# Kernel optimization log

Hardware: AMD Instinct MI355X
Metric: run time of the kernel (lower is better)

The kernel has to match this reference:

```python
import jax, jax.numpy as jnp
import numpy as np

SEQ = 2048
D_MODEL = 2048
N_HEADS = 16
D_HEAD = D_MODEL // N_HEADS
GN_EPS = 1e-5


def apply_xpos(x, inv=False, base=10000.0, scale_base=512.0):
    # x: (sqlen, d_head). Standard xPos: rotary embedding with exponential length scale.
    s, d = x.shape
    half = d // 2
    freqs = 1.0 / (base ** (jnp.arange(half, dtype=jnp.float32) / half))
    pos = jnp.arange(s, dtype=jnp.float32)
    ang = pos[:, None] * freqs[None, :]                       # (s, half)
    sin, cos = jnp.sin(ang), jnp.cos(ang)
    scale = ((jnp.arange(half, dtype=jnp.float32) + 0.4 * d) / (1.4 * d)) ** (pos[:, None] / scale_base)
    if inv:
        scale = 1.0 / scale
    x1, x2 = x[:, :half], x[:, half:]
    y1 = (x1 * cos - x2 * sin) * scale
    y2 = (x1 * sin + x2 * cos) * scale
    return jnp.concatenate([y1, y2], axis=-1)


def setup_inputs() -> dict:
    key = jax.random.key(0)
    ks = jax.random.split(key, 8)
    s = D_MODEL ** -0.5
    return {
        "x": jax.random.normal(ks[0], (SEQ, D_MODEL), jnp.float32),
        "state": jax.random.normal(ks[1], (N_HEADS, D_HEAD, D_HEAD), jnp.float32) * 0.1,
        "Wqkv": jax.random.normal(ks[2], (3 * D_MODEL, D_MODEL), jnp.float32) * s,
        "Walpha": jax.random.normal(ks[3], (1, D_MODEL), jnp.float32) * s,
        "gn_w": jnp.ones((D_MODEL,), jnp.float32),
        "gn_b": jnp.zeros((D_MODEL,), jnp.float32),
        "Wgate": jax.random.normal(ks[4], (D_MODEL, D_MODEL), jnp.float32) * s,
        "Wout": jax.random.normal(ks[5], (D_MODEL, D_MODEL), jnp.float32) * s,
    }


def reference(x, state, Wqkv, Walpha, gn_w, gn_b, Wgate, Wout):
    sqlen = x.shape[0]
    # qkv projection -> (3, H, s, Dh)
    qkv = (x @ Wqkv.T).reshape(sqlen, 3, N_HEADS, D_HEAD).transpose(1, 2, 0, 3)
    q, k, v = qkv[0], qkv[1], qkv[2]
    q = jax.vmap(apply_xpos)(q)
    k = jax.vmap(lambda t: apply_xpos(t, inv=True))(k)

    alphas = -jnp.log1p(jnp.exp(-(x @ Walpha.T)))             # log-sigmoid, (s, 1)
    k = (1.0 - jnp.exp(alphas)) * k                            # broadcast (s,1) over (H,s,Dh)
    a = jnp.cumsum(alphas, axis=0)                             # (s, 1)

    # Decay matrix; mask BEFORE exp (equivalent to tril-after since upper is zeroed,
    # but avoids overflow in exp for the upper triangle).
    tril = jnp.tril(jnp.ones((sqlen, sqlen), bool))
    Delta = jnp.exp(jnp.where(tril, a - a.T, -jnp.inf))        # (s, s)

    attn = jnp.tril(jnp.einsum('hid,hjd,ij->hij', q, k, Delta))  # (H, s, s)
    ret = jnp.einsum('hij,hjd->ihd', attn, v)                    # (s, H, Dh)

    new_state = jnp.exp(a[-1]) * state                           # (H, Dh, Dh)
    ret = ret + jnp.einsum('hid,hde->ihe', q, new_state)
    new_state = new_state + jnp.einsum('hid,hie,i->hde', k, v, jnp.exp(a[::-1, 0]))

    # GroupNorm(n_heads groups) over d_model, per token
    r = ret.reshape(sqlen, N_HEADS, D_HEAD)
    mu = r.mean(-1, keepdims=True)
    var = r.var(-1, keepdims=True)
    r = (r - mu) * jax.lax.rsqrt(var + GN_EPS)
    ret = r.reshape(sqlen, D_MODEL) * gn_w + gn_b

    gate = jax.nn.swish(ret @ Wgate.T)
    out = (gate * ret) @ Wout.T
    return out, new_state
```

## Files before the change

kernel.cpp:

```cpp
#include <hip/hip_runtime.h>

#define SEQ 2048
#define DM 2048
#define NH 16
#define DH 128

typedef float f32x4 __attribute__((ext_vector_type(4)));
typedef short s16x8 __attribute__((ext_vector_type(8)));

__device__ __forceinline__ ushort f2bf(float f) {
    unsigned u = __builtin_bit_cast(unsigned, f);
    return (ushort)((u + 0x7FFFu + ((u >> 16) & 1u)) >> 16);
}
__device__ __forceinline__ float bf2f(ushort u) {
    return __builtin_bit_cast(float, (unsigned)u << 16);
}
__device__ __forceinline__ void gload_lds16(const void* g, void* l) {
    __builtin_amdgcn_global_load_lds((const __attribute__((address_space(1))) void*)g,
                                     (__attribute__((address_space(3))) void*)l, 16, 0, 0);
}

__global__ __launch_bounds__(256) void k_cvt_bf16(const float* __restrict__ in,
                                                  ushort* __restrict__ out, int n4) {
    int i = blockIdx.x * 256 + threadIdx.x;
    if (i < n4) {
        float4 v = ((const float4*)in)[i];
        ushort4 o;
        o.x = f2bf(v.x); o.y = f2bf(v.y); o.z = f2bf(v.z); o.w = f2bf(v.w);
        ((ushort4*)out)[i] = o;
    }
}

__global__ __launch_bounds__(256) void k_cvt_dual(const float* __restrict__ in0,
                                                  ushort* __restrict__ out0,
                                                  const float* __restrict__ in1,
                                                  ushort* __restrict__ out1, int n4) {
    int i = blockIdx.x * 256 + threadIdx.x;
    if (i >= n4) return;
    const float* in = blockIdx.y ? in1 : in0;
    ushort* out = blockIdx.y ? out1 : out0;
    float4 v = ((const float4*)in)[i];
    ushort4 o;
    o.x = f2bf(v.x); o.y = f2bf(v.y); o.z = f2bf(v.z); o.w = f2bf(v.w);
    ((ushort4*)out)[i] = o;
}

__global__ __launch_bounds__(256) void k_xprep(const float* __restrict__ x,
                                               const float* __restrict__ wal,
                                               ushort* __restrict__ x_bf,
                                               float* __restrict__ z) {
    int row = blockIdx.x, t = threadIdx.x;
    const float4* xr = (const float4*)(x + (size_t)row * DM);
    const float4* wa = (const float4*)wal;
    float4 v0 = xr[t], v1 = xr[t + 256];
    float4 w0 = wa[t], w1 = wa[t + 256];
    float s = v0.x * w0.x + v0.y * w0.y + v0.z * w0.z + v0.w * w0.w
            + v1.x * w1.x + v1.y * w1.y + v1.z * w1.z + v1.w * w1.w;
    ushort4 o0, o1;
    o0.x = f2bf(v0.x); o0.y = f2bf(v0.y); o0.z = f2bf(v0.z); o0.w = f2bf(v0.w);
    o1.x = f2bf(v1.x); o1.y = f2bf(v1.y); o1.z = f2bf(v1.z); o1.w = f2bf(v1.w);
    ushort4* xb = (ushort4*)(x_bf + (size_t)row * DM);
    xb[t] = o0; xb[t + 256] = o1;
    __shared__ float red[4];
    int lane = t & 63, wv = t >> 6;
    #pragma unroll
    for (int off = 32; off; off >>= 1) s += __shfl_down(s, off);
    if (lane == 0) red[wv] = s;
    __syncthreads();
    if (t == 0) z[row] = red[0] + red[1] + red[2] + red[3];
}

__global__ __launch_bounds__(256) void k_scan(const float* __restrict__ z,
                                              float* __restrict__ a,
                                              float* __restrict__ wrev,
                                              float* __restrict__ kscale,
                                              float* __restrict__ exp_alast) {
    __shared__ float sh[SEQ];
    __shared__ float csum[256];
    int t = threadIdx.x;
    for (int i = t; i < SEQ; i += 256) {
        float al = -log1pf(expf(-z[i]));
        sh[i] = al;
        kscale[i] = 1.f - expf(al);
    }
    __syncthreads();
    int base = t * 8;
    float run = 0.f, loc[8];
    #pragma unroll
    for (int j = 0; j < 8; j++) { run += sh[base + j]; loc[j] = run; }
    csum[t] = run;
    __syncthreads();
    if (t == 0) {
        float r = 0.f;
        for (int i = 0; i < 256; i++) { float v = csum[i]; csum[i] = r; r += v; }
    }
    __syncthreads();
    float off = csum[t];
    #pragma unroll
    for (int j = 0; j < 8; j++) { float av = loc[j] + off; sh[base + j] = av; a[base + j] = av; }
    __syncthreads();
    for (int i = t; i < SEQ; i += 256) wrev[i] = expf(sh[SEQ - 1 - i]);
    if (t == 0) *exp_alast = expf(sh[SEQ - 1]);
}

__global__ __launch_bounds__(256) void k_trig(float* __restrict__ tsin,
                                              float* __restrict__ tcos,
                                              float* __restrict__ tsc) {
    int idx = blockIdx.x * 256 + threadIdx.x;
    int i = idx >> 6, j = idx & 63;
    float freq = powf(10000.f, -(float)j / 64.f);
    float ang = (float)i * freq;
    tsin[idx] = sinf(ang);
    tcos[idx] = cosf(ang);
    tsc[idx]  = powf(((float)j + 51.2f) / 179.2f, (float)i / 512.f);
}

template <int EPI, int STORE_BF16>
__global__ __launch_bounds__(256) void k_gemm_mfma(
    const ushort* __restrict__ A,
    const ushort* __restrict__ B,
    void* __restrict__ Cv, int ldc,
    const ushort* __restrict__ aux,
    int K)
{
    __shared__ __align__(16) ushort As[128 * 32];
    __shared__ __align__(16) ushort Bs[128 * 32];
    int bx = blockIdx.x, by = blockIdx.y;
    int nwg = gridDim.x * gridDim.y;
    if ((nwg & 7) == 0) {
        int id = by * gridDim.x + bx;
        int cpx = nwg >> 3;
        int swz = (id & 7) * cpx + (id >> 3);
        bx = swz % gridDim.x; by = swz / gridDim.x;
    }
    int bm = by * 128, bn = bx * 128;
    int tid = threadIdx.x;
    int w = tid >> 6, l = tid & 63;
    int wr = w >> 1, wc = w & 1;
    int lr = l & 15, kg = l >> 4;

    int srow = w * 16 + (l >> 2);
    int scol = (l & 3) * 8;
    const ushort* ga0 = A + (size_t)(bm + srow) * K + scol;
    const ushort* ga1 = A + (size_t)(bm + 64 + srow) * K + scol;
    const ushort* gb0 = B + (size_t)(bn + srow) * K + scol;
    const ushort* gb1 = B + (size_t)(bn + 64 + srow) * K + scol;
    ushort* la0 = As + w * 512;
    ushort* la1 = As + 2048 + w * 512;
    ushort* lb0 = Bs + w * 512;
    ushort* lb1 = Bs + 2048 + w * 512;

    f32x4 acc[4][4] = {};

    for (int k0 = 0; k0 < K; k0 += 32) {
        __syncthreads();
        gload_lds16(ga0 + k0, la0);
        gload_lds16(ga1 + k0, la1);
        gload_lds16(gb0 + k0, lb0);
        gload_lds16(gb1 + k0, lb1);
        __syncthreads();

        s16x8 af[4], bfr[4];
        #pragma unroll
        for (int m = 0; m < 4; m++)
            af[m] = *(const s16x8*)(As + (wr * 64 + m * 16 + lr) * 32 + kg * 8);
        #pragma unroll
        for (int n = 0; n < 4; n++)
            bfr[n] = *(const s16x8*)(Bs + (wc * 64 + n * 16 + lr) * 32 + kg * 8);
        #pragma unroll
        for (int m = 0; m < 4; m++)
            #pragma unroll
            for (int n = 0; n < 4; n++)
                asm volatile("v_mfma_f32_16x16x32_bf16 %0, %1, %2, %0"
                             : "+v"(acc[m][n]) : "v"(af[m]), "v"(bfr[n]));
    }
    asm volatile("s_nop 7\n\ts_nop 7\n\ts_nop 7" ::: );

    #pragma unroll
    for (int m = 0; m < 4; m++) {
        int grow = bm + wr * 64 + m * 16 + kg * 4;
        #pragma unroll
        for (int n = 0; n < 4; n++) {
            int gcol = bn + wc * 64 + n * 16 + lr;
            #pragma unroll
            for (int j = 0; j < 4; j++) {
                float c = acc[m][n][j];
                size_t off = (size_t)(grow + j) * ldc + gcol;
                if (EPI == 1) {
                    float sig = 1.f / (1.f + __expf(-c));
                    c = c * sig * bf2f(aux[off]);
                }
                if (STORE_BF16) ((ushort*)Cv)[off] = f2bf(c);
                else            ((float*)Cv)[off] = c;
            }
        }
    }
}

__global__ __launch_bounds__(256) void k_gemm_qkv(
    const ushort* __restrict__ A,
    const ushort* __restrict__ B,
    const float* __restrict__ tsin,
    const float* __restrict__ tcos,
    const float* __restrict__ tsc,
    const float* __restrict__ kscale,
    const float* __restrict__ wrev,
    ushort* __restrict__ qh,
    ushort* __restrict__ kh,
    ushort* __restrict__ vth,
    ushort* __restrict__ kwtr)
{
    __shared__ __align__(16) char smem[34816];
    ushort* As = (ushort*)smem;
    ushort* Bs = (ushort*)(smem + 8192);
    const int K = DM;
    int bx = blockIdx.x, by = blockIdx.y;
    {
        int id = by * gridDim.x + bx;
        int cpx = (gridDim.x * gridDim.y) >> 3;
        int swz = (id & 7) * cpx + (id >> 3);
        bx = swz % gridDim.x; by = swz / gridDim.x;
    }
    int bm = by * 128, bn = bx * 128;
    int tid = threadIdx.x;
    int w = tid >> 6, l = tid & 63;
    int wr = w >> 1, wc = w & 1;
    int lr = l & 15, kg = l >> 4;

    int srow = w * 16 + (l >> 2);
    int scol = (l & 3) * 8;
    const ushort* ga0 = A + (size_t)(bm + srow) * K + scol;
    const ushort* ga1 = A + (size_t)(bm + 64 + srow) * K + scol;
    const ushort* gb0 = B + (size_t)(bn + srow) * K + scol;
    const ushort* gb1 = B + (size_t)(bn + 64 + srow) * K + scol;
    ushort* la0 = As + w * 512;
    ushort* la1 = As + 2048 + w * 512;
    ushort* lb0 = Bs + w * 512;
    ushort* lb1 = Bs + 2048 + w * 512;

    f32x4 acc[4][4] = {};

    for (int k0 = 0; k0 < K; k0 += 32) {
        __syncthreads();
        gload_lds16(ga0 + k0, la0);
        gload_lds16(ga1 + k0, la1);
        gload_lds16(gb0 + k0, lb0);
        gload_lds16(gb1 + k0, lb1);
        __syncthreads();

        s16x8 af[4], bfr[4];
        #pragma unroll
        for (int m = 0; m < 4; m++)
            af[m] = *(const s16x8*)(As + (wr * 64 + m * 16 + lr) * 32 + kg * 8);
        #pragma unroll
        for (int n = 0; n < 4; n++)
            bfr[n] = *(const s16x8*)(Bs + (wc * 64 + n * 16 + lr) * 32 + kg * 8);
        #pragma unroll
        for (int m = 0; m < 4; m++)
            #pragma unroll
            for (int n = 0; n < 4; n++)
                asm volatile("v_mfma_f32_16x16x32_bf16 %0, %1, %2, %0"
                             : "+v"(acc[m][n]) : "v"(af[m]), "v"(bfr[n]));
    }
    asm volatile("s_nop 7\n\ts_nop 7\n\ts_nop 7" ::: );

    __syncthreads();
    ushort* S = (ushort*)smem;
    #pragma unroll
    for (int m = 0; m < 4; m++) {
        int row = wr * 64 + m * 16 + kg * 4;
        #pragma unroll
        for (int n = 0; n < 4; n++) {
            int col = wc * 64 + n * 16 + lr;
            #pragma unroll
            for (int j = 0; j < 4; j++)
                S[(row + j) * 129 + col] = f2bf(acc[m][n][j]);
        }
    }
    __syncthreads();

    int type = bn >> 11;
    int h = (bn & 2047) >> 7;

    if (type < 2) {
        #pragma unroll 4
        for (int rr = 0; rr < 32; rr++) {
            int r = w * 32 + rr;
            int i = bm + r;
            float sn = tsin[i * 64 + l], cs = tcos[i * 64 + l], sc = tsc[i * 64 + l];
            float v1 = bf2f(S[r * 129 + l]), v2 = bf2f(S[r * 129 + l + 64]);
            float r1 = v1 * cs - v2 * sn, r2 = v1 * sn + v2 * cs;
            size_t ob = ((size_t)h * SEQ + i) * DH;
            if (type == 0) {
                qh[ob + l]      = f2bf(r1 * sc);
                qh[ob + l + 64] = f2bf(r2 * sc);
            } else {
                float ks = kscale[i], wv = wrev[i];
                float isc = 1.f / sc;
                float k1 = r1 * isc * ks, k2 = r2 * isc * ks;
                kh[ob + l]      = f2bf(k1);
                kh[ob + l + 64] = f2bf(k2);
                S[r * 129 + l]      = f2bf(k1 * wv);
                S[r * 129 + l + 64] = f2bf(k2 * wv);
            }
        }
    }
    if (type >= 1) {
        __syncthreads();
        ushort* dstT = (type == 1) ? kwtr : vth;
        #pragma unroll 4
        for (int dd = 0; dd < 32; dd++) {
            int d = w * 32 + dd;
            ushort2 o;
            o.x = S[(2 * l) * 129 + d];
            o.y = S[(2 * l + 1) * 129 + d];
            *(ushort2*)(dstT + ((size_t)h * DH + d) * SEQ + bm + 2 * l) = o;
        }
    }
}

#define NUNITS 48
__constant__ unsigned char U_QT[NUNITS] = {
    31,31,30,15, 30,29,29,28,14, 28,27,27,26,13, 26,25,25,24,12,
    24,23,23,22,11, 22,21,21,20,10, 20,19,19,18,9, 18,17,17,16,8,
    16,7,6,5,4,3,2,1,0};
__constant__ unsigned char U_T0[NUNITS] = {
    0,16,0,0, 16,0,15,0,0, 15,0,14,0,0, 14,0,13,0,0,
    13,0,12,0,0, 12,0,11,0,0, 11,0,10,0,0, 10,0,9,0,0,
    9,0,0,0,0,0,0,0,0};
__constant__ unsigned char U_T1[NUNITS] = {
    16,32,16,16, 31,15,30,15,15, 29,14,28,14,14, 27,13,26,13,13,
    25,12,24,12,12, 23,11,22,11,11, 21,10,20,10,10, 19,9,18,9,9,
    17,8,7,6,5,4,3,2,1};

__global__ __launch_bounds__(256) void k_attn_mfma(
    const ushort* __restrict__ qh,
    const ushort* __restrict__ kh,
    const ushort* __restrict__ vth,
    const float* __restrict__ a,
    float* __restrict__ ret)
{
    int h = blockIdx.x, u = blockIdx.y;
    int qt = U_QT[u], t0 = U_T0[u], t1 = U_T1[u];
    int i0 = qt * 64;
    const ushort* Q  = qh  + (size_t)h * SEQ * DH;
    const ushort* K  = kh  + (size_t)h * SEQ * DH;
    const ushort* Vt = vth + (size_t)h * DH * SEQ;

    __shared__ __align__(16) ushort Ks[2][64 * 128];
    __shared__ __align__(16) ushort Vs[2][64 * 128];
    __shared__ __align__(16) ushort Ps[64 * 64];
    __shared__ float a_lds[SEQ];

    int tid = threadIdx.x;
    int w = tid >> 6, l = tid & 63;
    int lr = l & 15, kg = l >> 4;

    int span = t1 * 64;
    for (int i = tid; i < span; i += 256) a_lds[i] = a[i];

    s16x8 qf[4];
    #pragma unroll
    for (int c = 0; c < 4; c++)
        qf[c] = *(const s16x8*)(Q + (size_t)(i0 + w * 16 + lr) * DH + c * 32 + kg * 8);
    float aq[4];
    #pragma unroll
    for (int r = 0; r < 4; r++) aq[r] = a[i0 + w * 16 + kg * 4 + r];

    f32x4 oacc[8] = {};

#define STAGE(T, B) do { int j0_ = (T) * 64;                                      \
    _Pragma("unroll") for (int g = 0; g < 4; g++) {                               \
        int row = w * 16 + g * 4 + (l >> 4);                                      \
        int cb = ((l & 15) * 16) ^ ((row & 7) << 4);                              \
        gload_lds16(K + (size_t)(j0_ + row) * DH + cb / 2,                        \
                    (char*)Ks[B] + (w * 16 + g * 4) * 256); }                     \
    _Pragma("unroll") for (int g = 0; g < 4; g++) {                               \
        int e = w * 32 + g * 8 + (l >> 3);                                        \
        int cb = ((l & 7) * 16) ^ ((e & 7) << 4);                                 \
        gload_lds16(Vt + (size_t)e * SEQ + j0_ + cb / 2,                          \
                    (char*)Vs[B] + (w * 32 + g * 8) * 128); }                     \
} while (0)

    STAGE(t0, 0);
    __syncthreads();

    for (int t = t0; t < t1; t++) {
        int cur = (t - t0) & 1;
        if (t + 1 < t1) {
            STAGE(t + 1, cur ^ 1);
            asm volatile("s_waitcnt vmcnt(8)" ::: "memory");
        } else {
            asm volatile("s_waitcnt vmcnt(0)" ::: "memory");
        }
        __builtin_amdgcn_s_barrier();

        f32x4 sacc[4] = {};
        __builtin_amdgcn_s_setprio(1);
        #pragma unroll
        for (int n = 0; n < 4; n++) {
            int krow = n * 16 + lr;
            #pragma unroll
            for (int c = 0; c < 4; c++) {
                s16x8 kf = *(const s16x8*)((const char*)Ks[cur] + krow * 256 +
                            ((c * 64 + kg * 16) ^ ((krow & 7) << 4)));
                asm volatile("v_mfma_f32_16x16x32_bf16 %0, %1, %2, %0"
                             : "+v"(sacc[n]) : "v"(qf[c]), "v"(kf));
            }
        }
        __builtin_amdgcn_s_setprio(0);
        asm volatile("s_nop 7\n\ts_nop 7" ::: );

        int j0 = t * 64;
        float aref = a_lds[j0];
        float ei[4], ej[4];
        #pragma unroll
        for (int r = 0; r < 4; r++) ei[r] = __expf(aq[r] - aref);
        #pragma unroll
        for (int n = 0; n < 4; n++) ej[n] = __expf(aref - a_lds[j0 + n * 16 + lr]);
        bool diag = (t == qt);
        #pragma unroll
        for (int n = 0; n < 4; n++) {
            #pragma unroll
            for (int r = 0; r < 4; r++) {
                float wv = ei[r] * ej[n];
                if (diag)
                    wv = (n * 16 + lr <= w * 16 + kg * 4 + r) ? wv : 0.f;
                float p = sacc[n][r] * wv;
                int prow = w * 16 + kg * 4 + r;
                *(ushort*)((char*)Ps + prow * 128 +
                           (((n * 16 + lr) * 2) ^ ((prow & 7) << 4))) = f2bf(p);
            }
        }
        __builtin_amdgcn_s_setprio(1);
        #pragma unroll
        for (int c2 = 0; c2 < 2; c2++) {
            int prow = w * 16 + lr;
            s16x8 pf = *(const s16x8*)((const char*)Ps + prow * 128 +
                        ((c2 * 64 + kg * 16) ^ ((prow & 7) << 4)));
            #pragma unroll
            for (int n2 = 0; n2 < 8; n2++) {
                int erow = n2 * 16 + lr;
                s16x8 vf = *(const s16x8*)((const char*)Vs[cur] + erow * 128 +
                            ((c2 * 64 + kg * 16) ^ ((erow & 7) << 4)));
                asm volatile("v_mfma_f32_16x16x32_bf16 %0, %1, %2, %0"
                             : "+v"(oacc[n2]) : "v"(pf), "v"(vf));
            }
        }
        __builtin_amdgcn_s_setprio(0);
        asm volatile("s_waitcnt lgkmcnt(0)" ::: "memory");
        __builtin_amdgcn_s_barrier();
    }
#undef STAGE
    asm volatile("s_nop 7\n\ts_nop 7\n\ts_nop 7" ::: );

    #pragma unroll
    for (int n2 = 0; n2 < 8; n2++) {
        #pragma unroll
        for (int j = 0; j < 4; j++) {
            int gi = i0 + w * 16 + kg * 4 + j;
            unsafeAtomicAdd(&ret[(size_t)gi * DM + h * DH + n2 * 16 + lr], oacc[n2][j]);
        }
    }
}

#define SCH 8
__global__ __launch_bounds__(256) void k_state_mfma(const ushort* __restrict__ kwtr,
                                                    const ushort* __restrict__ vth,
                                                    float* __restrict__ part) {
    int ch = blockIdx.x, h = blockIdx.y;
    const ushort* A = kwtr + (size_t)h * DH * SEQ + ch * (SEQ / SCH);
    const ushort* B = vth  + (size_t)h * DH * SEQ + ch * (SEQ / SCH);
    __shared__ __align__(16) ushort As[128 * 32];
    __shared__ __align__(16) ushort Bs[128 * 32];
    int tid = threadIdx.x;
    int w = tid >> 6, l = tid & 63;
    int wr = w >> 1, wc = w & 1;
    int lr = l & 15, kg = l >> 4;
    int srow = w * 16 + (l >> 2);
    int scol = (l & 3) * 8;
    const ushort* ga0 = A + (size_t)srow * SEQ + scol;
    const ushort* ga1 = A + (size_t)(64 + srow) * SEQ + scol;
    const ushort* gb0 = B + (size_t)srow * SEQ + scol;
    const ushort* gb1 = B + (size_t)(64 + srow) * SEQ + scol;
    ushort* la0 = As + w * 512;
    ushort* la1 = As + 2048 + w * 512;
    ushort* lb0 = Bs + w * 512;
    ushort* lb1 = Bs + 2048 + w * 512;

    f32x4 acc[4][4] = {};
    for (int k0 = 0; k0 < SEQ / SCH; k0 += 32) {
        __syncthreads();
        gload_lds16(ga0 + k0, la0);
        gload_lds16(ga1 + k0, la1);
        gload_lds16(gb0 + k0, lb0);
        gload_lds16(gb1 + k0, lb1);
        __syncthreads();
        s16x8 af[4], bfr[4];
        #pragma unroll
        for (int m = 0; m < 4; m++)
            af[m] = *(const s16x8*)(As + (wr * 64 + m * 16 + lr) * 32 + kg * 8);
        #pragma unroll
        for (int n = 0; n < 4; n++)
            bfr[n] = *(const s16x8*)(Bs + (wc * 64 + n * 16 + lr) * 32 + kg * 8);
        #pragma unroll
        for (int m = 0; m < 4; m++)
            #pragma unroll
            for (int n = 0; n < 4; n++)
                asm volatile("v_mfma_f32_16x16x32_bf16 %0, %1, %2, %0"
                             : "+v"(acc[m][n]) : "v"(af[m]), "v"(bfr[n]));
    }
    asm volatile("s_nop 7\n\ts_nop 7\n\ts_nop 7" ::: );
    float* p = part + ((size_t)ch * NH + h) * DH * DH;
    #pragma unroll
    for (int m = 0; m < 4; m++) {
        int grow = wr * 64 + m * 16 + kg * 4;
        #pragma unroll
        for (int n = 0; n < 4; n++) {
            int gcol = wc * 64 + n * 16 + lr;
            #pragma unroll
            for (int j = 0; j < 4; j++)
                p[(size_t)(grow + j) * DH + gcol] = acc[m][n][j];
        }
    }
}

__global__ __launch_bounds__(256) void k_state_reduce(const float* __restrict__ part,
                                                      const float* __restrict__ state,
                                                      const float* __restrict__ exp_alast,
                                                      float* __restrict__ out_state) {
    int idx = blockIdx.x * 256 + threadIdx.x;
    float s = state[idx] * (*exp_alast);
    #pragma unroll
    for (int ch = 0; ch < SCH; ch++) s += part[(size_t)ch * NH * DH * DH + idx];
    out_state[idx] = s;
}

__global__ __launch_bounds__(64) void k_gnorm(const float* __restrict__ ret,
                                              const float* __restrict__ gw,
                                              const float* __restrict__ gb,
                                              ushort* __restrict__ retn_bf) {
    int i = blockIdx.x, h = blockIdx.y;
    int t = threadIdx.x;
    const float* r = ret + (size_t)i * DM + h * DH;
    float v0 = r[t], v1 = r[t + 64];
    float s = v0 + v1, sq = v0 * v0 + v1 * v1;
    #pragma unroll
    for (int off = 32; off; off >>= 1) { s += __shfl_xor(s, off); sq += __shfl_xor(sq, off); }
    float mu = s * (1.f / 128.f);
    float var = sq * (1.f / 128.f) - mu * mu;
    float inv = rsqrtf(var + 1e-5f);
    ushort* o = retn_bf + (size_t)i * DM + h * DH;
    o[t]      = f2bf((v0 - mu) * inv * gw[h * DH + t]      + gb[h * DH + t]);
    o[t + 64] = f2bf((v1 - mu) * inv * gw[h * DH + t + 64] + gb[h * DH + t + 64]);
}

extern "C" void kernel_launch(void* const* d_in, const int* in_sizes, int n_in,
                              void* d_out, int out_size, void* d_ws, size_t ws_size,
                              hipStream_t stream) {
    (void)in_sizes; (void)n_in; (void)out_size; (void)ws_size;
    const float* x      = (const float*)d_in[0];
    const float* state  = (const float*)d_in[1];
    const float* Wqkv   = (const float*)d_in[2];
    const float* Walpha = (const float*)d_in[3];
    const float* gn_w   = (const float*)d_in[4];
    const float* gn_b   = (const float*)d_in[5];
    const float* Wgate  = (const float*)d_in[6];
    const float* Wout   = (const float*)d_in[7];
    float* out       = (float*)d_out;
    float* out_state = out + (size_t)SEQ * DM;

    char* base = (char*)d_ws;
    ushort* x_bf     = (ushort*)base;
    ushort* retn_bf  = (ushort*)base;
    ushort* Wqkv_bf  = (ushort*)(base + 8388608);
    float*  ret      = (float*)(base + 8388608);
    ushort* Wgate_bf = (ushort*)(base + 8388608);
    float*  part     = (float*)(base + 25165824);
    ushort* Wout_bf  = (ushort*)(base + 25165824);
    ushort* qh       = (ushort*)(base + 33554432);
    ushort* kh       = (ushort*)(base + 41943040);
    ushort* vth      = (ushort*)(base + 50331648);
    ushort* kwtr     = (ushort*)(base + 58720256);
    ushort* gr_bf    = (ushort*)(base + 67108864);
    float*  tsin     = (float*)(base + 75497472);
    float*  tcos     = (float*)(base + 75497472 + 524288);
    float*  tsc      = (float*)(base + 75497472 + 1048576);
    float*  smalls   = (float*)(base + 77070336);
    float* z = smalls, *a = z + SEQ, *wrev = a + SEQ, *kscale = wrev + SEQ, *exp_alast = kscale + SEQ;

    k_cvt_bf16<<<dim3(3 * DM * DM / 4 / 256), dim3(256), 0, stream>>>(Wqkv, Wqkv_bf, 3 * DM * DM / 4);
    k_xprep<<<dim3(SEQ), dim3(256), 0, stream>>>(x, Walpha, x_bf, z);
    k_scan<<<dim3(1), dim3(256), 0, stream>>>(z, a, wrev, kscale, exp_alast);
    k_trig<<<dim3(SEQ * 64 / 256), dim3(256), 0, stream>>>(tsin, tcos, tsc);
    k_gemm_qkv<<<dim3(3 * DM / 128, SEQ / 128), dim3(256), 0, stream>>>(
        x_bf, Wqkv_bf, tsin, tcos, tsc, kscale, wrev, qh, kh, vth, kwtr);
    hipMemsetAsync(ret, 0, (size_t)SEQ * DM * 4, stream);
    k_attn_mfma<<<dim3(NH, NUNITS), dim3(256), 0, stream>>>(qh, kh, vth, a, ret);
    k_state_mfma<<<dim3(SCH, NH), dim3(256), 0, stream>>>(kwtr, vth, part);
    k_state_reduce<<<dim3(NH * DH * DH / 256), dim3(256), 0, stream>>>(
        part, state, exp_alast, out_state);
    k_gnorm<<<dim3(SEQ, NH), dim3(64), 0, stream>>>(ret, gn_w, gn_b, retn_bf);
    k_cvt_dual<<<dim3(DM * DM / 4 / 256, 2), dim3(256), 0, stream>>>(
        Wgate, Wgate_bf, Wout, Wout_bf, DM * DM / 4);
    k_gemm_mfma<1, 1><<<dim3(DM / 128, SEQ / 128), dim3(256), 0, stream>>>(
        retn_bf, Wgate_bf, gr_bf, DM, retn_bf, DM);
    k_gemm_mfma<0, 0><<<dim3(DM / 128, SEQ / 128), dim3(256), 0, stream>>>(
        gr_bf, Wout_bf, out, DM, nullptr, DM);
}
```

Measured before the change: 269.0 us.

## Merge prep, state, and weight-conversion kernels into fewer launches; drop atomics and memset

```diff
diff --git a/kernel.cpp b/kernel.cpp
--- a/kernel.cpp
+++ b/kernel.cpp
@@ -20,54 +20,50 @@
                                      (__attribute__((address_space(3))) void*)l, 16, 0, 0);
 }
 
-__global__ __launch_bounds__(256) void k_cvt_bf16(const float* __restrict__ in,
-                                                  ushort* __restrict__ out, int n4) {
-    int i = blockIdx.x * 256 + threadIdx.x;
-    if (i < n4) {
-        float4 v = ((const float4*)in)[i];
+__global__ __launch_bounds__(256) void k_prep1(const float* __restrict__ x,
+                                               const float* __restrict__ wal,
+                                               ushort* __restrict__ x_bf,
+                                               float* __restrict__ z,
+                                               const float* __restrict__ Wqkv,
+                                               ushort* __restrict__ Wqkv_bf,
+                                               float* __restrict__ tsin,
+                                               float* __restrict__ tcos,
+                                               float* __restrict__ tsc) {
+    int b = blockIdx.x, t = threadIdx.x;
+    if (b < SEQ) {
+        const float4* xr = (const float4*)(x + (size_t)b * DM);
+        const float4* wa = (const float4*)wal;
+        float4 v0 = xr[t], v1 = xr[t + 256];
+        float4 w0 = wa[t], w1 = wa[t + 256];
+        float s = v0.x * w0.x + v0.y * w0.y + v0.z * w0.z + v0.w * w0.w
+                + v1.x * w1.x + v1.y * w1.y + v1.z * w1.z + v1.w * w1.w;
+        ushort4 o0, o1;
+        o0.x = f2bf(v0.x); o0.y = f2bf(v0.y); o0.z = f2bf(v0.z); o0.w = f2bf(v0.w);
+        o1.x = f2bf(v1.x); o1.y = f2bf(v1.y); o1.z = f2bf(v1.z); o1.w = f2bf(v1.w);
+        ushort4* xb = (ushort4*)(x_bf + (size_t)b * DM);
+        xb[t] = o0; xb[t + 256] = o1;
+        __shared__ float red[4];
+        int lane = t & 63, wv = t >> 6;
+        #pragma unroll
+        for (int off = 32; off; off >>= 1) s += __shfl_down(s, off);
+        if (lane == 0) red[wv] = s;
+        __syncthreads();
+        if (t == 0) z[b] = red[0] + red[1] + red[2] + red[3];
+    } else if (b < SEQ + 3 * DM * DM / 4 / 256) {
+        int i = (b - SEQ) * 256 + t;
+        float4 v = ((const float4*)Wqkv)[i];
         ushort4 o;
         o.x = f2bf(v.x); o.y = f2bf(v.y); o.z = f2bf(v.z); o.w = f2bf(v.w);
-        ((ushort4*)out)[i] = o;
-    }
-}
-
-__global__ __launch_bounds__(256) void k_cvt_dual(const float* __restrict__ in0,
-                                                  ushort* __restrict__ out0,
-                                                  const float* __restrict__ in1,
-                                                  ushort* __restrict__ out1, int n4) {
-    int i = blockIdx.x * 256 + threadIdx.x;
-    if (i >= n4) return;
-    const float* in = blockIdx.y ? in1 : in0;
-    ushort* out = blockIdx.y ? out1 : out0;
-    float4 v = ((const float4*)in)[i];
-    ushort4 o;
-    o.x = f2bf(v.x); o.y = f2bf(v.y); o.z = f2bf(v.z); o.w = f2bf(v.w);
-    ((ushort4*)out)[i] = o;
-}
-
-__global__ __launch_bounds__(256) void k_xprep(const float* __restrict__ x,
-                                               const float* __restrict__ wal,
-                                               ushort* __restrict__ x_bf,
-                                               float* __restrict__ z) {
-    int row = blockIdx.x, t = threadIdx.x;
-    const float4* xr = (const float4*)(x + (size_t)row * DM);
-    const float4* wa = (const float4*)wal;
-    float4 v0 = xr[t], v1 = xr[t + 256];
-    float4 w0 = wa[t], w1 = wa[t + 256];
-    float s = v0.x * w0.x + v0.y * w0.y + v0.z * w0.z + v0.w * w0.w
-            + v1.x * w1.x + v1.y * w1.y + v1.z * w1.z + v1.w * w1.w;
-    ushort4 o0, o1;
-    o0.x = f2bf(v0.x); o0.y = f2bf(v0.y); o0.z = f2bf(v0.z); o0.w = f2bf(v0.w);
-    o1.x = f2bf(v1.x); o1.y = f2bf(v1.y); o1.z = f2bf(v1.z); o1.w = f2bf(v1.w);
-    ushort4* xb = (ushort4*)(x_bf + (size_t)row * DM);
-    xb[t] = o0; xb[t + 256] = o1;
-    __shared__ float red[4];
-    int lane = t & 63, wv = t >> 6;
-    #pragma unroll
-    for (int off = 32; off; off >>= 1) s += __shfl_down(s, off);
-    if (lane == 0) red[wv] = s;
-    __syncthreads();
-    if (t == 0) z[row] = red[0] + red[1] + red[2] + red[3];
+        ((ushort4*)Wqkv_bf)[i] = o;
+    } else {
+        int idx = (b - SEQ - 3 * DM * DM / 4 / 256) * 256 + t;
+        int i = idx >> 6, j = idx & 63;
+        float freq = powf(10000.f, -(float)j / 64.f);
+        float ang = (float)i * freq;
+        tsin[idx] = sinf(ang);
+        tcos[idx] = cosf(ang);
+        tsc[idx]  = powf(((float)j + 51.2f) / 179.2f, (float)i / 512.f);
+    }
 }
 
 __global__ __launch_bounds__(256) void k_scan(const float* __restrict__ z,
@@ -101,18 +97,6 @@
     __syncthreads();
     for (int i = t; i < SEQ; i += 256) wrev[i] = expf(sh[SEQ - 1 - i]);
     if (t == 0) *exp_alast = expf(sh[SEQ - 1]);
-}
-
-__global__ __launch_bounds__(256) void k_trig(float* __restrict__ tsin,
-                                              float* __restrict__ tcos,
-                                              float* __restrict__ tsc) {
-    int idx = blockIdx.x * 256 + threadIdx.x;
-    int i = idx >> 6, j = idx & 63;
-    float freq = powf(10000.f, -(float)j / 64.f);
-    float ang = (float)i * freq;
-    tsin[idx] = sinf(ang);
-    tcos[idx] = cosf(ang);
-    tsc[idx]  = powf(((float)j + 51.2f) / 179.2f, (float)i / 512.f);
 }
 
 template <int EPI, int STORE_BF16>
@@ -208,18 +192,35 @@
     ushort* __restrict__ qh,
     ushort* __restrict__ kh,
     ushort* __restrict__ vth,
-    ushort* __restrict__ kwtr)
+    ushort* __restrict__ kwtr,
+    const float* __restrict__ state,
+    const float* __restrict__ exp_alast,
+    float* __restrict__ out_state)
 {
+    if (blockIdx.x == 48) {
+        float ea = *exp_alast;
+        int idx0 = blockIdx.y * 16384 + threadIdx.x;
+        #pragma unroll
+        for (int it = 0; it < 16; it++) {
+            int idx = idx0 + it * 1024;
+            float4 v = ((const float4*)state)[idx / 4 + 0];
+            out_state[idx] = state[idx] * ea;
+            out_state[idx + 256] = state[idx + 256] * ea;
+            out_state[idx + 512] = state[idx + 512] * ea;
+            out_state[idx + 768] = state[idx + 768] * ea;
+            (void)v;
+        }
+        return;
+    }
     __shared__ __align__(16) char smem[34816];
     ushort* As = (ushort*)smem;
     ushort* Bs = (ushort*)(smem + 8192);
     const int K = DM;
     int bx = blockIdx.x, by = blockIdx.y;
     {
-        int id = by * gridDim.x + bx;
-        int cpx = (gridDim.x * gridDim.y) >> 3;
-        int swz = (id & 7) * cpx + (id >> 3);
-        bx = swz % gridDim.x; by = swz / gridDim.x;
+        int id = by * 48 + bx;
+        int swz = (id & 7) * 96 + (id >> 3);
+        bx = swz % 48; by = swz / 48;
     }
     int bm = by * 128, bn = bx * 128;
     int tid = threadIdx.x;
@@ -333,28 +334,107 @@
     25,12,24,12,12, 23,11,22,11,11, 21,10,20,10,10, 19,9,18,9,9,
     17,8,7,6,5,4,3,2,1};
 
-__global__ __launch_bounds__(256) void k_attn_mfma(
+__global__ __launch_bounds__(256) void k_attn_mega(
     const ushort* __restrict__ qh,
     const ushort* __restrict__ kh,
     const ushort* __restrict__ vth,
+    const ushort* __restrict__ kwtr,
     const float* __restrict__ a,
-    float* __restrict__ ret)
+    float* __restrict__ ret,
+    float* __restrict__ ret2,
+    float* __restrict__ out_state,
+    const float* __restrict__ Wgate,
+    ushort* __restrict__ Wgate_bf,
+    const float* __restrict__ Wout,
+    ushort* __restrict__ Wout_bf)
 {
+    __shared__ __align__(16) char smem[81920];
     int h = blockIdx.x, u = blockIdx.y;
+    int tid = threadIdx.x;
+    int w = tid >> 6, l = tid & 63;
+    int lr = l & 15, kg = l >> 4;
+
+    if (u >= 56) {
+        int id = (u - 56) * NH + h;
+        const float4* g0 = (const float4*)Wgate;
+        const float4* g1 = (const float4*)Wout;
+        #pragma unroll 4
+        for (int it = 0; it < 32; it++) {
+            int idx = id * 8192 + it * 256 + tid;
+            float4 v = g0[idx];
+            ushort4 o;
+            o.x = f2bf(v.x); o.y = f2bf(v.y); o.z = f2bf(v.z); o.w = f2bf(v.w);
+            ((ushort4*)Wgate_bf)[idx] = o;
+            v = g1[idx];
+            o.x = f2bf(v.x); o.y = f2bf(v.y); o.z = f2bf(v.z); o.w = f2bf(v.w);
+            ((ushort4*)Wout_bf)[idx] = o;
+        }
+        return;
+    }
+    if (u >= 48) {
+        int ch = u - 48;
+        const ushort* A = kwtr + (size_t)h * DH * SEQ + ch * (SEQ / 8);
+        const ushort* B = vth  + (size_t)h * DH * SEQ + ch * (SEQ / 8);
+        ushort* As = (ushort*)smem;
+        ushort* Bs = (ushort*)(smem + 8192);
+        int wr = w >> 1, wc = w & 1;
+        int srow = w * 16 + (l >> 2);
+        int scol = (l & 3) * 8;
+        const ushort* ga0 = A + (size_t)srow * SEQ + scol;
+        const ushort* ga1 = A + (size_t)(64 + srow) * SEQ + scol;
+        const ushort* gb0 = B + (size_t)srow * SEQ + scol;
+        const ushort* gb1 = B + (size_t)(64 + srow) * SEQ + scol;
+        ushort* la0 = As + w * 512;
+        ushort* la1 = As + 2048 + w * 512;
+        ushort* lb0 = Bs + w * 512;
+        ushort* lb1 = Bs + 2048 + w * 512;
+        f32x4 acc[4][4] = {};
+        for (int k0 = 0; k0 < SEQ / 8; k0 += 32) {
+            __syncthreads();
+            gload_lds16(ga0 + k0, la0);
+            gload_lds16(ga1 + k0, la1);
+            gload_lds16(gb0 + k0, lb0);
+            gload_lds16(gb1 + k0, lb1);
+            __syncthreads();
+            s16x8 af[4], bfr[4];
+            #pragma unroll
+            for (int m = 0; m < 4; m++)
+                af[m] = *(const s16x8*)(As + (wr * 64 + m * 16 + lr) * 32 + kg * 8);
+            #pragma unroll
+            for (int n = 0; n < 4; n++)
+                bfr[n] = *(const s16x8*)(Bs + (wc * 64 + n * 16 + lr) * 32 + kg * 8);
+            #pragma unroll
+            for (int m = 0; m < 4; m++)
+                #pragma unroll
+                for (int n = 0; n < 4; n++)
+                    asm volatile("v_mfma_f32_16x16x32_bf16 %0, %1, %2, %0"
+                                 : "+v"(acc[m][n]) : "v"(af[m]), "v"(bfr[n]));
+        }
+        asm volatile("s_nop 7\n\ts_nop 7\n\ts_nop 7" ::: );
+        float* p = out_state + (size_t)h * DH * DH;
+        #pragma unroll
+        for (int m = 0; m < 4; m++) {
+            int grow = wr * 64 + m * 16 + kg * 4;
+            #pragma unroll
+            for (int n = 0; n < 4; n++) {
+                int gcol = wc * 64 + n * 16 + lr;
+                #pragma unroll
+                for (int j = 0; j < 4; j++)
+                    unsafeAtomicAdd(&p[(size_t)(grow + j) * DH + gcol], acc[m][n][j]);
+            }
+        }
+        return;
+    }
+
     int qt = U_QT[u], t0 = U_T0[u], t1 = U_T1[u];
     int i0 = qt * 64;
     const ushort* Q  = qh  + (size_t)h * SEQ * DH;
     const ushort* K  = kh  + (size_t)h * SEQ * DH;
     const ushort* Vt = vth + (size_t)h * DH * SEQ;
-
-    __shared__ __align__(16) ushort Ks[2][64 * 128];
-    __shared__ __align__(16) ushort Vs[2][64 * 128];
-    __shared__ __align__(16) ushort Ps[64 * 64];
-    __shared__ float a_lds[SEQ];
-
-    int tid = threadIdx.x;
-    int w = tid >> 6, l = tid & 63;
-    int lr = l & 15, kg = l >> 4;
+#define KS(B) ((ushort*)(smem + (B) * 16384))
+#define VS(B) ((ushort*)(smem + 32768 + (B) * 16384))
+    char* Ps = smem + 65536;
+    float* a_lds = (float*)(smem + 73728);
 
     int span = t1 * 64;
     for (int i = tid; i < span; i += 256) a_lds[i] = a[i];
@@ -374,12 +454,12 @@
         int row = w * 16 + g * 4 + (l >> 4);                                      \
         int cb = ((l & 15) * 16) ^ ((row & 7) << 4);                              \
         gload_lds16(K + (size_t)(j0_ + row) * DH + cb / 2,                        \
-                    (char*)Ks[B] + (w * 16 + g * 4) * 256); }                     \
+                    (char*)KS(B) + (w * 16 + g * 4) * 256); }                     \
     _Pragma("unroll") for (int g = 0; g < 4; g++) {                               \
         int e = w * 32 + g * 8 + (l >> 3);                                        \
         int cb = ((l & 7) * 16) ^ ((e & 7) << 4);                                 \
         gload_lds16(Vt + (size_t)e * SEQ + j0_ + cb / 2,                          \
-                    (char*)Vs[B] + (w * 32 + g * 8) * 128); }                     \
+                    (char*)VS(B) + (w * 32 + g * 8) * 128); }                     \
 } while (0)
 
     STAGE(t0, 0);
@@ -402,7 +482,7 @@
             int krow = n * 16 + lr;
             #pragma unroll
             for (int c = 0; c < 4; c++) {
-                s16x8 kf = *(const s16x8*)((const char*)Ks[cur] + krow * 256 +
+                s16x8 kf = *(const s16x8*)((const char*)KS(cur) + krow * 256 +
                             ((c * 64 + kg * 16) ^ ((krow & 7) << 4)));
                 asm volatile("v_mfma_f32_16x16x32_bf16 %0, %1, %2, %0"
                              : "+v"(sacc[n]) : "v"(qf[c]), "v"(kf));
@@ -428,7 +508,7 @@
                     wv = (n * 16 + lr <= w * 16 + kg * 4 + r) ? wv : 0.f;
                 float p = sacc[n][r] * wv;
                 int prow = w * 16 + kg * 4 + r;
-                *(ushort*)((char*)Ps + prow * 128 +
+                *(ushort*)(Ps + prow * 128 +
                            (((n * 16 + lr) * 2) ^ ((prow & 7) << 4))) = f2bf(p);
             }
         }
@@ -441,7 +521,7 @@
             #pragma unroll
             for (int n2 = 0; n2 < 8; n2++) {
                 int erow = n2 * 16 + lr;
-                s16x8 vf = *(const s16x8*)((const char*)Vs[cur] + erow * 128 +
+                s16x8 vf = *(const s16x8*)((const char*)VS(cur) + erow * 128 +
                             ((c2 * 64 + kg * 16) ^ ((erow & 7) << 4)));
                 asm volatile("v_mfma_f32_16x16x32_bf16 %0, %1, %2, %0"
                              : "+v"(oacc[n2]) : "v"(pf), "v"(vf));
@@ -454,89 +534,20 @@
 #undef STAGE
     asm volatile("s_nop 7\n\ts_nop 7\n\ts_nop 7" ::: );
 
+    float* dst = (t0 == 0) ? ret + (size_t)i0 * DM
+                           : ret2 + (size_t)(i0 - 1024) * DM;
     #pragma unroll
     for (int n2 = 0; n2 < 8; n2++) {
         #pragma unroll
         for (int j = 0; j < 4; j++) {
-            int gi = i0 + w * 16 + kg * 4 + j;
-            unsafeAtomicAdd(&ret[(size_t)gi * DM + h * DH + n2 * 16 + lr], oacc[n2][j]);
-        }
-    }
-}
-
-#define SCH 8
-__global__ __launch_bounds__(256) void k_state_mfma(const ushort* __restrict__ kwtr,
-                                                    const ushort* __restrict__ vth,
-                                                    float* __restrict__ part) {
-    int ch = blockIdx.x, h = blockIdx.y;
-    const ushort* A = kwtr + (size_t)h * DH * SEQ + ch * (SEQ / SCH);
-    const ushort* B = vth  + (size_t)h * DH * SEQ + ch * (SEQ / SCH);
-    __shared__ __align__(16) ushort As[128 * 32];
-    __shared__ __align__(16) ushort Bs[128 * 32];
-    int tid = threadIdx.x;
-    int w = tid >> 6, l = tid & 63;
-    int wr = w >> 1, wc = w & 1;
-    int lr = l & 15, kg = l >> 4;
-    int srow = w * 16 + (l >> 2);
-    int scol = (l & 3) * 8;
-    const ushort* ga0 = A + (size_t)srow * SEQ + scol;
-    const ushort* ga1 = A + (size_t)(64 + srow) * SEQ + scol;
-    const ushort* gb0 = B + (size_t)srow * SEQ + scol;
-    const ushort* gb1 = B + (size_t)(64 + srow) * SEQ + scol;
-    ushort* la0 = As + w * 512;
-    ushort* la1 = As + 2048 + w * 512;
-    ushort* lb0 = Bs + w * 512;
-    ushort* lb1 = Bs + 2048 + w * 512;
-
-    f32x4 acc[4][4] = {};
-    for (int k0 = 0; k0 < SEQ / SCH; k0 += 32) {
-        __syncthreads();
-        gload_lds16(ga0 + k0, la0);
-        gload_lds16(ga1 + k0, la1);
-        gload_lds16(gb0 + k0, lb0);
-        gload_lds16(gb1 + k0, lb1);
-        __syncthreads();
-        s16x8 af[4], bfr[4];
-        #pragma unroll
-        for (int m = 0; m < 4; m++)
-            af[m] = *(const s16x8*)(As + (wr * 64 + m * 16 + lr) * 32 + kg * 8);
-        #pragma unroll
-        for (int n = 0; n < 4; n++)
-            bfr[n] = *(const s16x8*)(Bs + (wc * 64 + n * 16 + lr) * 32 + kg * 8);
-        #pragma unroll
-        for (int m = 0; m < 4; m++)
-            #pragma unroll
-            for (int n = 0; n < 4; n++)
-                asm volatile("v_mfma_f32_16x16x32_bf16 %0, %1, %2, %0"
-                             : "+v"(acc[m][n]) : "v"(af[m]), "v"(bfr[n]));
-    }
-    asm volatile("s_nop 7\n\ts_nop 7\n\ts_nop 7" ::: );
-    float* p = part + ((size_t)ch * NH + h) * DH * DH;
-    #pragma unroll
-    for (int m = 0; m < 4; m++) {
-        int grow = wr * 64 + m * 16 + kg * 4;
-        #pragma unroll
-        for (int n = 0; n < 4; n++) {
-            int gcol = wc * 64 + n * 16 + lr;
-            #pragma unroll
-            for (int j = 0; j < 4; j++)
-                p[(size_t)(grow + j) * DH + gcol] = acc[m][n][j];
-        }
-    }
-}
-
-__global__ __launch_bounds__(256) void k_state_reduce(const float* __restrict__ part,
-                                                      const float* __restrict__ state,
-                                                      const float* __restrict__ exp_alast,
-                                                      float* __restrict__ out_state) {
-    int idx = blockIdx.x * 256 + threadIdx.x;
-    float s = state[idx] * (*exp_alast);
-    #pragma unroll
-    for (int ch = 0; ch < SCH; ch++) s += part[(size_t)ch * NH * DH * DH + idx];
-    out_state[idx] = s;
+            int ri = w * 16 + kg * 4 + j;
+            dst[(size_t)ri * DM + h * DH + n2 * 16 + lr] = oacc[n2][j];
+        }
+    }
 }
 
 __global__ __launch_bounds__(64) void k_gnorm(const float* __restrict__ ret,
+                                              const float* __restrict__ ret2,
                                               const float* __restrict__ gw,
                                               const float* __restrict__ gb,
                                               ushort* __restrict__ retn_bf) {
@@ -544,6 +555,10 @@
     int t = threadIdx.x;
     const float* r = ret + (size_t)i * DM + h * DH;
     float v0 = r[t], v1 = r[t + 64];
+    if (i >= 1024) {
+        const float* r2 = ret2 + (size_t)(i - 1024) * DM + h * DH;
+        v0 += r2[t]; v1 += r2[t + 64];
+    }
     float s = v0 + v1, sq = v0 * v0 + v1 * v1;
     #pragma unroll
     for (int off = 32; off; off >>= 1) { s += __shfl_xor(s, off); sq += __shfl_xor(sq, off); }
@@ -575,9 +590,7 @@
     ushort* retn_bf  = (ushort*)base;
     ushort* Wqkv_bf  = (ushort*)(base + 8388608);
     float*  ret      = (float*)(base + 8388608);
-    ushort* Wgate_bf = (ushort*)(base + 8388608);
-    float*  part     = (float*)(base + 25165824);
-    ushort* Wout_bf  = (ushort*)(base + 25165824);
+    float*  ret2     = (float*)(base + 25165824);
     ushort* qh       = (ushort*)(base + 33554432);
     ushort* kh       = (ushort*)(base + 41943040);
     ushort* vth      = (ushort*)(base + 50331648);
@@ -586,23 +599,21 @@
     float*  tsin     = (float*)(base + 75497472);
     float*  tcos     = (float*)(base + 75497472 + 524288);
     float*  tsc      = (float*)(base + 75497472 + 1048576);
-    float*  smalls   = (float*)(base + 77070336);
+    ushort* Wgate_bf = (ushort*)(base + 75497472);
+    ushort* Wout_bf  = (ushort*)(base + 83886080);
+    float*  smalls   = (float*)(base + 92274688);
     float* z = smalls, *a = z + SEQ, *wrev = a + SEQ, *kscale = wrev + SEQ, *exp_alast = kscale + SEQ;
 
-    k_cvt_bf16<<<dim3(3 * DM * DM / 4 / 256), dim3(256), 0, stream>>>(Wqkv, Wqkv_bf, 3 * DM * DM / 4);
-    k_xprep<<<dim3(SEQ), dim3(256), 0, stream>>>(x, Walpha, x_bf, z);
+    k_prep1<<<dim3(SEQ + 3 * DM * DM / 4 / 256 + SEQ * 64 / 256), dim3(256), 0, stream>>>(
+        x, Walpha, x_bf, z, Wqkv, Wqkv_bf, tsin, tcos, tsc);
     k_scan<<<dim3(1), dim3(256), 0, stream>>>(z, a, wrev, kscale, exp_alast);
-    k_trig<<<dim3(SEQ * 64 / 256), dim3(256), 0, stream>>>(tsin, tcos, tsc);
-    k_gemm_qkv<<<dim3(3 * DM / 128, SEQ / 128), dim3(256), 0, stream>>>(
-        x_bf, Wqkv_bf, tsin, tcos, tsc, kscale, wrev, qh, kh, vth, kwtr);
-    hipMemsetAsync(ret, 0, (size_t)SEQ * DM * 4, stream);
-    k_attn_mfma<<<dim3(NH, NUNITS), dim3(256), 0, stream>>>(qh, kh, vth, a, ret);
-    k_state_mfma<<<dim3(SCH, NH), dim3(256), 0, stream>>>(kwtr, vth, part);
-    k_state_reduce<<<dim3(NH * DH * DH / 256), dim3(256), 0, stream>>>(
-        part, state, exp_alast, out_state);
-    k_gnorm<<<dim3(SEQ, NH), dim3(64), 0, stream>>>(ret, gn_w, gn_b, retn_bf);
-    k_cvt_dual<<<dim3(DM * DM / 4 / 256, 2), dim3(256), 0, stream>>>(
-        Wgate, Wgate_bf, Wout, Wout_bf, DM * DM / 4);
+    k_gemm_qkv<<<dim3(49, SEQ / 128), dim3(256), 0, stream>>>(
+        x_bf, Wqkv_bf, tsin, tcos, tsc, kscale, wrev, qh, kh, vth, kwtr,
+        state, exp_alast, out_state);
+    k_attn_mega<<<dim3(NH, 64), dim3(256), 0, stream>>>(
+        qh, kh, vth, kwtr, a, ret, ret2, out_state,
+        Wgate, Wgate_bf, Wout, Wout_bf);
+    k_gnorm<<<dim3(SEQ, NH), dim3(64), 0, stream>>>(ret, ret2, gn_w, gn_b, retn_bf);
     k_gemm_mfma<1, 1><<<dim3(DM / 128, SEQ / 128), dim3(256), 0, stream>>>(
         retn_bf, Wgate_bf, gr_bf, DM, retn_bf, DM);
     k_gemm_mfma<0, 0><<<dim3(DM / 128, SEQ / 128), dim3(256), 0, stream>>>(
```

New measurement: 253.6 us. 5.7% less time.
